# Optimization experiments

Measured on AMD Instinct MI355X. Metric: run time of the kernel, lower is better.

Reference implementation:

```python
import jax, jax.numpy as jnp
import numpy as np

N, C, D, H, W = 1, 32, 64, 192, 160


def affine_grid_3d(theta, size):
    # PyTorch F.affine_grid 3D, align_corners=True convention.
    n, c, d, h, w = size
    z = jnp.linspace(-1.0, 1.0, d)
    y = jnp.linspace(-1.0, 1.0, h)
    x = jnp.linspace(-1.0, 1.0, w)
    zz, yy, xx = jnp.meshgrid(z, y, x, indexing='ij')          # [D,H,W]
    base = jnp.stack([xx, yy, zz, jnp.ones_like(xx)], axis=-1)  # [D,H,W,4]
    return jnp.einsum('dhwk,nck->ndhwc', base, theta)           # [N,D,H,W,3] (x,y,z)


def _gather_corner(vol, zi, yi, xi):
    # vol: [C,D,H,W]; zi/yi/xi: [D,H,W] int32. Zero padding outside.
    c, d, h, w = vol.shape
    valid = (zi >= 0) & (zi < d) & (yi >= 0) & (yi < h) & (xi >= 0) & (xi < w)
    zc = jnp.clip(zi, 0, d - 1)
    yc = jnp.clip(yi, 0, h - 1)
    xc = jnp.clip(xi, 0, w - 1)
    flat = vol.reshape(c, d * h * w)
    idx = (zc * h + yc) * w + xc
    vals = jnp.take(flat, idx.reshape(-1), axis=1).reshape(c, *zi.shape)
    return vals * valid[None].astype(vol.dtype)


def grid_sample_3d(inp, grid):
    # Trilinear grid_sample, zeros padding, align_corners=True.
    n, c, d, h, w = inp.shape
    x = (grid[..., 0] + 1.0) * 0.5 * (w - 1)
    y = (grid[..., 1] + 1.0) * 0.5 * (h - 1)
    z = (grid[..., 2] + 1.0) * 0.5 * (d - 1)
    x0 = jnp.floor(x).astype(jnp.int32); x1 = x0 + 1
    y0 = jnp.floor(y).astype(jnp.int32); y1 = y0 + 1
    z0 = jnp.floor(z).astype(jnp.int32); z1 = z0 + 1
    wx = (x - x0.astype(x.dtype))
    wy = (y - y0.astype(y.dtype))
    wz = (z - z0.astype(z.dtype))

    def sample_one(vol, z0, z1, y0, y1, x0, x1, wz, wy, wx):
        out = jnp.zeros((vol.shape[0],) + wz.shape, dtype=vol.dtype)
        for zi, wzc in ((z0, 1.0 - wz), (z1, wz)):
            for yi, wyc in ((y0, 1.0 - wy), (y1, wy)):
                for xi, wxc in ((x0, 1.0 - wx), (x1, wx)):
                    out = out + _gather_corner(vol, zi, yi, xi) * (wzc * wyc * wxc)[None]
        return out

    return jax.vmap(sample_one)(inp, z0, z1, y0, y1, x0, x1, wz, wy, wx)


def setup_inputs() -> dict:
    key = jax.random.key(0)
    k1, k2 = jax.random.split(key)
    inp = jax.random.normal(k1, (N, C, D, H, W), dtype=jnp.float32)
    identity = jnp.asarray([1, 0, 0, 0, 0, 1, 0, 0, 0, 0, 1, 0], dtype=jnp.float32)
    theta = identity + 0.1 * jax.random.normal(k2, (12,), dtype=jnp.float32)
    return {"input": inp, "theta": theta}


def reference(input, theta):
    th = theta.reshape(1, 3, 4)
    grid = affine_grid_3d(th, input.shape)       # [N,D,H,W,3]
    out = grid_sample_3d(input, grid)            # [N,C,D,H,W]
    return jnp.transpose(out, (0, 4, 3, 1, 2))   # [N,W,H,C,D]
```

## Files before the change

### kernel.cpp

```cpp
#include <hip/hip_runtime.h>

constexpr int W_ = 160;
constexpr int H_ = 192;
constexpr int D_ = 64;
constexpr int C_ = 32;
constexpr int HW_  = H_ * W_;
constexpr int DHWi = D_ * HW_;
constexpr int CD   = C_ * D_;

constexpr int TW = 32, TH = 12, TD = 16;
constexpr int NWT = W_ / TW;
constexpr int NHT = H_ / TH;
constexpr int NDT = D_ / TD;
constexpr int QPP = NWT * NHT;
constexpr int CPX = C_ / 8;
constexpr int NPH = CPX * NDT;
constexpr int LDS_BYTES = 53248;
constexpr int LSTR = 20;

typedef float f4_t __attribute__((ext_vector_type(4)));
typedef float f2_t __attribute__((ext_vector_type(2)));

__global__ void __launch_bounds__(256)
affine_grid_sample_kernel(const float* __restrict__ inp,
                          const float* __restrict__ th,
                          float* __restrict__ out)
{
    extern __shared__ float smem[];

    const int t   = threadIdx.x;
    const int bid = blockIdx.x;
    const int xcd = bid & 7;
    int r = bid >> 3;
    const int phase = r / QPP;
    const int q     = r - phase * QPP;
    const int c  = xcd * CPX + (phase >> 2);
    const int dt = phase & 3;
    const int hs = q / NWT;
    const int wt = q - hs * NWT;
    const int w0 = wt * TW, h0 = hs * TH, d0 = dt * TD;

    const float th0=th[0], th1=th[1], th2 =th[2],  th3 =th[3];
    const float th4=th[4], th5=th[5], th6 =th[6],  th7 =th[7];
    const float th8=th[8], th9=th[9], th10=th[10], th11=th[11];

    const float* __restrict__ pc = inp + (size_t)c * DHWi;

    const int w = w0 + (t & 31);
    const int g = t >> 5;
    const float xx = fmaf((float)w, 2.0f / (W_ - 1), -1.0f);

    float kzx[2], kzy[2], kzz[2];
    #pragma unroll
    for (int kk = 0; kk < 2; ++kk) {
        const int d = d0 + 2 * g + kk;
        const float zz = fmaf((float)d, 2.0f / (D_ - 1), -1.0f);
        kzx[kk] = fmaf(th2,  zz, th3);
        kzy[kk] = fmaf(th6,  zz, th7);
        kzz[kk] = fmaf(th10, zz, th11);
    }

    #pragma unroll 1
    for (int hl = 0; hl < TH; ++hl) {
        const int h = h0 + hl;
        const float yy = fmaf((float)h, 2.0f / (H_ - 1), -1.0f);
        float* __restrict__ L = smem + (hl & 1) * (TW * LSTR);

        unsigned o[2][8];
        float u0a[2], u1a[2], v0a[2], v1a[2], s0a[2], s1a[2];
        #pragma unroll
        for (int kk = 0; kk < 2; ++kk) {
            const float px = (fmaf(th0, xx, fmaf(th1, yy, kzx[kk])) + 1.0f) * (0.5f * (W_ - 1));
            const float py = (fmaf(th4, xx, fmaf(th5, yy, kzy[kk])) + 1.0f) * (0.5f * (H_ - 1));
            const float pz = (fmaf(th8, xx, fmaf(th9, yy, kzz[kk])) + 1.0f) * (0.5f * (D_ - 1));
            const float fx = floorf(px), fy = floorf(py), fz = floorf(pz);
            const int ix0 = (int)fx, iy0 = (int)fy, iz0 = (int)fz;
            const int ix1 = ix0 + 1, iy1 = iy0 + 1, iz1 = iz0 + 1;
            const float wx = px - fx, wy = py - fy, wz = pz - fz;
            u0a[kk] = (ix0 >= 0 && ix0 < W_) ? (1.0f - wx) : 0.0f;
            u1a[kk] = (ix1 >= 0 && ix1 < W_) ? wx          : 0.0f;
            v0a[kk] = (iy0 >= 0 && iy0 < H_) ? (1.0f - wy) : 0.0f;
            v1a[kk] = (iy1 >= 0 && iy1 < H_) ? wy          : 0.0f;
            s0a[kk] = (iz0 >= 0 && iz0 < D_) ? (1.0f - wz) : 0.0f;
            s1a[kk] = (iz1 >= 0 && iz1 < D_) ? wz          : 0.0f;
            const int cx0 = min(max(ix0, 0), W_ - 1), cx1 = min(max(ix1, 0), W_ - 1);
            const int cy0 = min(max(iy0, 0), H_ - 1), cy1 = min(max(iy1, 0), H_ - 1);
            const int cz0 = min(max(iz0, 0), D_ - 1), cz1 = min(max(iz1, 0), D_ - 1);
            const unsigned o00 = (unsigned)(cz0 * HW_ + cy0 * W_);
            const unsigned o01 = (unsigned)(cz0 * HW_ + cy1 * W_);
            const unsigned o10 = (unsigned)(cz1 * HW_ + cy0 * W_);
            const unsigned o11 = (unsigned)(cz1 * HW_ + cy1 * W_);
            o[kk][0] = o00 + (unsigned)cx0;
            o[kk][1] = o00 + (unsigned)cx1;
            o[kk][2] = o01 + (unsigned)cx0;
            o[kk][3] = o01 + (unsigned)cx1;
            o[kk][4] = o10 + (unsigned)cx0;
            o[kk][5] = o10 + (unsigned)cx1;
            o[kk][6] = o11 + (unsigned)cx0;
            o[kk][7] = o11 + (unsigned)cx1;
        }

        float b[2][8];
        #pragma unroll
        for (int kk = 0; kk < 2; ++kk)
            #pragma unroll
            for (int j = 0; j < 8; ++j)
                b[kk][j] = pc[o[kk][j]];

        f2_t val;
        #pragma unroll
        for (int kk = 0; kk < 2; ++kk) {
            const float r00 = u0a[kk] * b[kk][0] + u1a[kk] * b[kk][1];
            const float r01 = u0a[kk] * b[kk][2] + u1a[kk] * b[kk][3];
            const float r10 = u0a[kk] * b[kk][4] + u1a[kk] * b[kk][5];
            const float r11 = u0a[kk] * b[kk][6] + u1a[kk] * b[kk][7];
            const float e0 = v0a[kk] * r00 + v1a[kk] * r01;
            const float e1 = v0a[kk] * r10 + v1a[kk] * r11;
            val[kk] = s0a[kk] * e0 + s1a[kk] * e1;
        }
        *(f2_t*)&L[(t & 31) * LSTR + 2 * g] = val;

        __syncthreads();

        if (t < 128) {
            const int w2 = t >> 2;
            const int qd = t & 3;
            const f4_t v = *(const f4_t*)&L[w2 * LSTR + 4 * qd];
            float* ob = out + ((size_t)(w0 + w2) * H_ + h) * CD
                            + (size_t)c * D_ + d0 + 4 * qd;
            __builtin_nontemporal_store(v, (f4_t*)ob);
        }
    }
}

extern "C" void kernel_launch(void* const* d_in, const int* in_sizes, int n_in,
                              void* d_out, int out_size, void* d_ws, size_t ws_size,
                              hipStream_t stream)
{
    const float* inp = (const float*)d_in[0];
    const float* th  = (const float*)d_in[1];
    float* out = (float*)d_out;

    hipLaunchKernelGGL(affine_grid_sample_kernel, dim3(8 * NPH * QPP), dim3(256),
                       LDS_BYTES, stream, inp, th, out);
}
```

Baseline: 709.1 us.

## Compute four depth samples per thread and store directly, dropping LDS transpose

Remaps threads so each computes four consecutive depth outputs for one (w,h) and writes them as a single 16-byte nontemporal store. This removes the shared-memory staging buffer and the per-row __syncthreads, and two half-blocks now process alternating h rows. It also sets launch bounds to 4 blocks per CU and shrinks the dynamic LDS request. In exchange, each thread holds 32 gathered values and more address state, which raises register pressure. The stores are also less coalesced across the wave (16 lanes per row instead of full contiguous segments).

```diff
diff --git a/kernel.cpp b/kernel.cpp
--- a/kernel.cpp
+++ b/kernel.cpp
@@ -15,13 +15,11 @@
 constexpr int QPP = NWT * NHT;
 constexpr int CPX = C_ / 8;
 constexpr int NPH = CPX * NDT;
-constexpr int LDS_BYTES = 53248;
-constexpr int LSTR = 20;
+constexpr int LDS_BYTES = 36864;
 
 typedef float f4_t __attribute__((ext_vector_type(4)));
-typedef float f2_t __attribute__((ext_vector_type(2)));
 
-__global__ void __launch_bounds__(256)
+__global__ void __launch_bounds__(256, 4)
 affine_grid_sample_kernel(const float* __restrict__ inp,
                           const float* __restrict__ th,
                           float* __restrict__ out)
@@ -40,49 +38,54 @@
     const int wt = q - hs * NWT;
     const int w0 = wt * TW, h0 = hs * TH, d0 = dt * TD;
 
+    if (bid < 0) smem[t] = 0.0f;
+
     const float th0=th[0], th1=th[1], th2 =th[2],  th3 =th[3];
     const float th4=th[4], th5=th[5], th6 =th[6],  th7 =th[7];
     const float th8=th[8], th9=th[9], th10=th[10], th11=th[11];
 
     const float* __restrict__ pc = inp + (size_t)c * DHWi;
 
-    const int w = w0 + (t & 31);
-    const int g = t >> 5;
+    const int wl = t & 15;
+    const int dq = (t >> 4) & 3;
+    const int wh = (t >> 6) & 1;
+    const int hp = t >> 7;
+    const int w  = w0 + wh * 16 + wl;
     const float xx = fmaf((float)w, 2.0f / (W_ - 1), -1.0f);
 
-    float kzx[2], kzy[2], kzz[2];
+    float kzx[4], kzy[4], kzz[4];
     #pragma unroll
-    for (int kk = 0; kk < 2; ++kk) {
-        const int d = d0 + 2 * g + kk;
+    for (int k = 0; k < 4; ++k) {
+        const int d = d0 + 4 * dq + k;
         const float zz = fmaf((float)d, 2.0f / (D_ - 1), -1.0f);
-        kzx[kk] = fmaf(th2,  zz, th3);
-        kzy[kk] = fmaf(th6,  zz, th7);
-        kzz[kk] = fmaf(th10, zz, th11);
+        kzx[k] = fmaf(th2,  zz, th3);
+        kzy[k] = fmaf(th6,  zz, th7);
+        kzz[k] = fmaf(th10, zz, th11);
     }
 
+    float* const ob = out + ((size_t)w * H_ + h0) * CD + (size_t)c * D_ + d0 + 4 * dq;
+
     #pragma unroll 1
-    for (int hl = 0; hl < TH; ++hl) {
-        const int h = h0 + hl;
-        const float yy = fmaf((float)h, 2.0f / (H_ - 1), -1.0f);
-        float* __restrict__ L = smem + (hl & 1) * (TW * LSTR);
+    for (int hh = hp; hh < TH; hh += 2) {
+        const float yy = fmaf((float)(h0 + hh), 2.0f / (H_ - 1), -1.0f);
 
-        unsigned o[2][8];
-        float u0a[2], u1a[2], v0a[2], v1a[2], s0a[2], s1a[2];
+        unsigned o[4][8];
+        float u0a[4], u1a[4], v0a[4], v1a[4], s0a[4], s1a[4];
         #pragma unroll
-        for (int kk = 0; kk < 2; ++kk) {
-            const float px = (fmaf(th0, xx, fmaf(th1, yy, kzx[kk])) + 1.0f) * (0.5f * (W_ - 1));
-            const float py = (fmaf(th4, xx, fmaf(th5, yy, kzy[kk])) + 1.0f) * (0.5f * (H_ - 1));
-            const float pz = (fmaf(th8, xx, fmaf(th9, yy, kzz[kk])) + 1.0f) * (0.5f * (D_ - 1));
+        for (int k = 0; k < 4; ++k) {
+            const float px = (fmaf(th0, xx, fmaf(th1, yy, kzx[k])) + 1.0f) * (0.5f * (W_ - 1));
+            const float py = (fmaf(th4, xx, fmaf(th5, yy, kzy[k])) + 1.0f) * (0.5f * (H_ - 1));
+            const float pz = (fmaf(th8, xx, fmaf(th9, yy, kzz[k])) + 1.0f) * (0.5f * (D_ - 1));
             const float fx = floorf(px), fy = floorf(py), fz = floorf(pz);
             const int ix0 = (int)fx, iy0 = (int)fy, iz0 = (int)fz;
             const int ix1 = ix0 + 1, iy1 = iy0 + 1, iz1 = iz0 + 1;
             const float wx = px - fx, wy = py - fy, wz = pz - fz;
-            u0a[kk] = (ix0 >= 0 && ix0 < W_) ? (1.0f - wx) : 0.0f;
-            u1a[kk] = (ix1 >= 0 && ix1 < W_) ? wx          : 0.0f;
-            v0a[kk] = (iy0 >= 0 && iy0 < H_) ? (1.0f - wy) : 0.0f;
-            v1a[kk] = (iy1 >= 0 && iy1 < H_) ? wy          : 0.0f;
-            s0a[kk] = (iz0 >= 0 && iz0 < D_) ? (1.0f - wz) : 0.0f;
-            s1a[kk] = (iz1 >= 0 && iz1 < D_) ? wz          : 0.0f;
+            u0a[k] = (ix0 >= 0 && ix0 < W_) ? (1.0f - wx) : 0.0f;
+            u1a[k] = (ix1 >= 0 && ix1 < W_) ? wx          : 0.0f;
+            v0a[k] = (iy0 >= 0 && iy0 < H_) ? (1.0f - wy) : 0.0f;
+            v1a[k] = (iy1 >= 0 && iy1 < H_) ? wy          : 0.0f;
+            s0a[k] = (iz0 >= 0 && iz0 < D_) ? (1.0f - wz) : 0.0f;
+            s1a[k] = (iz1 >= 0 && iz1 < D_) ? wz          : 0.0f;
             const int cx0 = min(max(ix0, 0), W_ - 1), cx1 = min(max(ix1, 0), W_ - 1);
             const int cy0 = min(max(iy0, 0), H_ - 1), cy1 = min(max(iy1, 0), H_ - 1);
             const int cz0 = min(max(iz0, 0), D_ - 1), cz1 = min(max(iz1, 0), D_ - 1);
@@ -90,46 +93,35 @@
             const unsigned o01 = (unsigned)(cz0 * HW_ + cy1 * W_);
             const unsigned o10 = (unsigned)(cz1 * HW_ + cy0 * W_);
             const unsigned o11 = (unsigned)(cz1 * HW_ + cy1 * W_);
-            o[kk][0] = o00 + (unsigned)cx0;
-            o[kk][1] = o00 + (unsigned)cx1;
-            o[kk][2] = o01 + (unsigned)cx0;
-            o[kk][3] = o01 + (unsigned)cx1;
-            o[kk][4] = o10 + (unsigned)cx0;
-            o[kk][5] = o10 + (unsigned)cx1;
-            o[kk][6] = o11 + (unsigned)cx0;
-            o[kk][7] = o11 + (unsigned)cx1;
+            o[k][0] = o00 + (unsigned)cx0;
+            o[k][1] = o00 + (unsigned)cx1;
+            o[k][2] = o01 + (unsigned)cx0;
+            o[k][3] = o01 + (unsigned)cx1;
+            o[k][4] = o10 + (unsigned)cx0;
+            o[k][5] = o10 + (unsigned)cx1;
+            o[k][6] = o11 + (unsigned)cx0;
+            o[k][7] = o11 + (unsigned)cx1;
         }
 
-        float b[2][8];
+        float b[4][8];
         #pragma unroll
-        for (int kk = 0; kk < 2; ++kk)
+        for (int k = 0; k < 4; ++k)
             #pragma unroll
             for (int j = 0; j < 8; ++j)
-                b[kk][j] = pc[o[kk][j]];
+                b[k][j] = pc[o[k][j]];
 
-        f2_t val;
+        f4_t val;
         #pragma unroll
-        for (int kk = 0; kk < 2; ++kk) {
-            const float r00 = u0a[kk] * b[kk][0] + u1a[kk] * b[kk][1];
-            const float r01 = u0a[kk] * b[kk][2] + u1a[kk] * b[kk][3];
-            const float r10 = u0a[kk] * b[kk][4] + u1a[kk] * b[kk][5];
-            const float r11 = u0a[kk] * b[kk][6] + u1a[kk] * b[kk][7];
-            const float e0 = v0a[kk] * r00 + v1a[kk] * r01;
-            const float e1 = v0a[kk] * r10 + v1a[kk] * r11;
-            val[kk] = s0a[kk] * e0 + s1a[kk] * e1;
+        for (int k = 0; k < 4; ++k) {
+            const float r00 = u0a[k] * b[k][0] + u1a[k] * b[k][1];
+            const float r01 = u0a[k] * b[k][2] + u1a[k] * b[k][3];
+            const float r10 = u0a[k] * b[k][4] + u1a[k] * b[k][5];
+            const float r11 = u0a[k] * b[k][6] + u1a[k] * b[k][7];
+            const float e0 = v0a[k] * r00 + v1a[k] * r01;
+            const float e1 = v0a[k] * r10 + v1a[k] * r11;
+            val[k] = s0a[k] * e0 + s1a[k] * e1;
         }
-        *(f2_t*)&L[(t & 31) * LSTR + 2 * g] = val;
-
-        __syncthreads();
-
-        if (t < 128) {
-            const int w2 = t >> 2;
-            const int qd = t & 3;
-            const f4_t v = *(const f4_t*)&L[w2 * LSTR + 4 * qd];
-            float* ob = out + ((size_t)(w0 + w2) * H_ + h) * CD
-                            + (size_t)c * D_ + d0 + 4 * qd;
-            __builtin_nontemporal_store(v, (f4_t*)ob);
-        }
+        __builtin_nontemporal_store(val, (f4_t*)(ob + (size_t)hh * CD));
     }
 }
 
```

Measured after the change: 719.9 us. No clear change (+1.5%).
